# Performance work log

Hardware: AMD Instinct MI355X
Metric: run time of the kernel (lower is better)

The kernel has to match this reference:

```python
import jax, jax.numpy as jnp
import numpy as np

B, N, K = 8, 2048, 32
WIDTH = 20.0      # histogram bin width in degrees
NUM_BINS = 9
EPS = 1e-12       # F.normalize eps


def _knn_idx(pts, k):
    """pts: (B,N,3) -> (B,N,k) indices of k nearest neighbors (incl. self).
    Matches dgcnn.pytorch knn: topk of negative squared distance."""
    d2 = jnp.sum(pts * pts, axis=-1)                       # (B,N)
    neg = 2.0 * jnp.einsum('bnd,bmd->bnm', pts, pts) - d2[:, :, None] - d2[:, None, :]
    _, idx = jax.lax.top_k(neg, k)                         # (B,N,k)
    return idx


def _gather_nn(feat, idx):
    """feat: (B,N,C), idx: (B,N,k) -> (B,N,k,C) per-batch gather."""
    return jax.vmap(lambda f, i: f[i])(feat, idx)


def setup_inputs() -> dict:
    key = jax.random.key(0)
    x = jax.random.normal(key, (B, 3, N), dtype=jnp.float32)
    return {"x": x, "k": K}


def reference(x, k):
    """Faithful JAX port of compute_hog_1x1. x: (B,3,N) -> (B,18,N)."""
    b, _, n = x.shape
    pts = jnp.transpose(x, (0, 2, 1))                      # (B,N,3)
    idx = _knn_idx(pts, k)                                 # (B,N,k)

    x_nn = _gather_nn(pts, idx)                            # (B,N,k,3)
    centered = x_nn - x_nn.mean(axis=2, keepdims=True)

    # Batched SVD; the original detaches (numpy round-trip) -> stop_gradient.
    _, s, vh = jnp.linalg.svd(centered, full_matrices=False)  # s:(B,N,3) vh:(B,N,3,3)
    vh = jax.lax.stop_gradient(vh)
    s = jax.lax.stop_gradient(jnp.sqrt(s))
    gradients = vh[:, :, 0]                                # (B,N,3) principal direction
    magnitudes = s[:, :, 0:1]                              # (B,N,1)

    g_nn = _gather_nn(gradients, idx)                      # (B,N,k,3)
    m_nn = _gather_nn(magnitudes, idx)                     # (B,N,k,1)

    rad2deg = 180.0 / np.pi
    zenith = jnp.arccos(g_nn[..., 2]) * rad2deg            # (B,N,k)
    azimuth = jnp.arctan(g_nn[..., 1] / g_nn[..., 0]) * rad2deg
    # .int() cast in torch truncates toward zero
    ang = jnp.stack([zenith, azimuth], axis=-1).astype(jnp.int32).astype(x.dtype)
    ang = jnp.where(ang < 0, ang + 180.0, ang)             # (B,N,k,2)

    bins = jnp.floor(ang / WIDTH - 0.5) % NUM_BINS         # (B,N,k,2) float
    first_centers = WIDTH * ((bins + 1.0) % NUM_BINS + 0.5)
    first_votes = m_nn * ((first_centers - ang) % 180.0) / WIDTH
    second_centers = WIDTH * (bins + 0.5)
    second_votes = m_nn * ((ang - second_centers) % 180.0) / WIDTH

    bi = bins.astype(jnp.int32)                            # (B,N,k,2)
    oh1 = jax.nn.one_hot(bi, NUM_BINS, dtype=x.dtype)      # (B,N,k,2,9)
    oh2 = jax.nn.one_hot((bi + 1) % NUM_BINS, NUM_BINS, dtype=x.dtype)
    # histogram[:, :, c] += first where bins==c; histogram[:, :, (c+1)%9] += second
    hist = (jnp.einsum('bnkc,bnkcq->bnqc', first_votes, oh1)
            + jnp.einsum('bnkc,bnkcq->bnqc', second_votes, oh2))  # (B,N,9,2)

    # F.normalize(p=2, dim=2)
    norm = jnp.sqrt(jnp.sum(hist * hist, axis=2, keepdims=True))
    hist = hist / jnp.maximum(norm, EPS)

    # torch .view(B, -1, N): flat row-major reinterpret -> (B,18,N)
    return hist.reshape(b, 2 * NUM_BINS, n)
```

## Files before the change

kernel.cpp:

```cpp
#include <hip/hip_runtime.h>
#include <math.h>

#define BB 8
#define NN 2048
#define KK 32

__device__ __forceinline__ float fadd(float a, float b){ return __fadd_rn(a, b); }
__device__ __forceinline__ float fsub(float a, float b){ return __fsub_rn(a, b); }
__device__ __forceinline__ float fmul(float a, float b){ return __fmul_rn(a, b); }
__device__ __forceinline__ float fdiv(float a, float b){ return __fdiv_rn(a, b); }
__device__ __forceinline__ float fsqrtf32(float a){ return __fsqrt_rn(a); }

__device__ float slapy2f(float x, float y) {
    float xa = fabsf(x), ya = fabsf(y);
    float w = fmaxf(xa, ya), z = fminf(xa, ya);
    if (z == 0.0f) return w;
    float q = fdiv(z, w);
    return fmul(w, fsqrtf32(fmaf(q, q, 1.0f)));
}

__device__ void slartgf(float f, float g, float& c, float& s, float& r) {
    if (g == 0.0f) { c = 1.0f; s = 0.0f; r = f; }
    else if (f == 0.0f) { c = 0.0f; s = copysignf(1.0f, g); r = fabsf(g); }
    else {
        float d = fsqrtf32(fmaf(f, f, fmul(g, g)));
        c = fdiv(fabsf(f), d);
        r = copysignf(d, f);
        s = fdiv(g, r);
    }
}

__device__ void slas2f(float f, float g, float h, float& ssmin, float& ssmax) {
    float fa = fabsf(f), ga = fabsf(g), ha = fabsf(h);
    float fhmn = fminf(fa, ha), fhmx = fmaxf(fa, ha);
    if (fhmn == 0.0f) {
        ssmin = 0.0f;
        if (fhmx == 0.0f) ssmax = ga;
        else {
            float mx = fmaxf(fhmx, ga), mn = fminf(fhmx, ga);
            float q = fdiv(mn, mx);
            ssmax = fmul(mx, fsqrtf32(fmaf(q, q, 1.0f)));
        }
    } else {
        if (ga < fhmx) {
            float as = fadd(1.0f, fdiv(fhmn, fhmx));
            float at = fdiv(fsub(fhmx, fhmn), fhmx);
            float q = fdiv(ga, fhmx); float au = fmul(q, q);
            float c = fdiv(2.0f, fadd(fsqrtf32(fmaf(as, as, au)),
                                      fsqrtf32(fmaf(at, at, au))));
            ssmin = fmul(fhmn, c); ssmax = fdiv(fhmx, c);
        } else {
            float au = fdiv(fhmx, ga);
            if (au == 0.0f) { ssmin = fdiv(fmul(fhmn, fhmx), ga); ssmax = ga; }
            else {
                float as = fadd(1.0f, fdiv(fhmn, fhmx));
                float at = fdiv(fsub(fhmx, fhmn), fhmx);
                float t1 = fmul(as, au), t2 = fmul(at, au);
                float c = fdiv(1.0f, fadd(fsqrtf32(fmaf(t1, t1, 1.0f)),
                                          fsqrtf32(fmaf(t2, t2, 1.0f))));
                ssmin = fmul(fmul(fhmn, c), au); ssmin = fadd(ssmin, ssmin);
                ssmax = fdiv(ga, fadd(c, c));
            }
        }
    }
}

__device__ void slasv2f(float f, float g, float h,
                        float& ssmin, float& ssmax,
                        float& snr, float& csr, float& snl, float& csl) {
    const float eps = 5.9604644775390625e-08f;
    float ft = f, fa = fabsf(f), ht = h, ha = fabsf(h);
    int pmax = 1;
    bool swp = (ha > fa);
    if (swp) { pmax = 3; float t = ft; ft = ht; ht = t; t = fa; fa = ha; ha = t; }
    float gt = g, ga = fabsf(gt);
    float clt = 0.f, crt = 0.f, slt = 0.f, srt = 0.f;
    if (ga == 0.0f) {
        ssmin = ha; ssmax = fa; clt = 1.0f; crt = 1.0f; slt = 0.0f; srt = 0.0f;
    } else {
        bool gasmal = true;
        if (ga > fa) {
            pmax = 2;
            if (fdiv(fa, ga) < eps) {
                gasmal = false;
                ssmax = ga;
                ssmin = (ha > 1.0f) ? fdiv(fa, fdiv(ga, ha)) : fmul(fdiv(fa, ga), ha);
                clt = 1.0f; slt = fdiv(ht, gt); srt = 1.0f; crt = fdiv(ft, gt);
            }
        }
        if (gasmal) {
            float dd = fsub(fa, ha);
            float l = (dd == fa) ? 1.0f : fdiv(dd, fa);
            float mm = fdiv(gt, ft);
            float t = fsub(2.0f, l);
            float m2 = fmul(mm, mm);
            float s = fsqrtf32(fmaf(t, t, m2));
            float r = (l == 0.0f) ? fabsf(mm) : fsqrtf32(fmaf(l, l, m2));
            float a = fmul(0.5f, fadd(s, r));
            ssmin = fdiv(ha, a);
            ssmax = fmul(fa, a);
            if (m2 == 0.0f) {
                t = (l == 0.0f) ? fmul(copysignf(2.0f, ft), copysignf(1.0f, gt))
                                : fadd(fdiv(gt, copysignf(dd, ft)), fdiv(mm, t));
            } else {
                t = fmul(fadd(fdiv(mm, fadd(s, t)), fdiv(mm, fadd(r, l))), fadd(1.0f, a));
            }
            float l2 = fsqrtf32(fmaf(t, t, 4.0f));
            crt = fdiv(2.0f, l2); srt = fdiv(t, l2);
            clt = fdiv(fmaf(srt, mm, crt), a);
            slt = fdiv(fmul(fdiv(ht, ft), srt), a);
        }
    }
    if (swp) { csl = srt; snl = crt; csr = slt; snr = clt; }
    else     { csl = clt; snl = slt; csr = crt; snr = srt; }
    float tsign = 0.0f;
    if (pmax == 1) tsign = fmul(fmul(copysignf(1.f, csr), copysignf(1.f, csl)), copysignf(1.f, f));
    if (pmax == 2) tsign = fmul(fmul(copysignf(1.f, snr), copysignf(1.f, csl)), copysignf(1.f, g));
    if (pmax == 3) tsign = fmul(fmul(copysignf(1.f, snr), copysignf(1.f, snl)), copysignf(1.f, h));
    ssmax = copysignf(fabsf(ssmax), tsign);
    ssmin = copysignf(fabsf(ssmin), fmul(tsign, fmul(copysignf(1.f, f), copysignf(1.f, h))));
}

__device__ __forceinline__ void rot_rowsf(float vt[4][4], int lo, int hi, float cc, float ss) {
    #pragma unroll
    for (int c = 1; c <= 3; ++c) {
        float t = vt[hi][c];
        vt[hi][c] = fmaf(cc, t, -fmul(ss, vt[lo][c]));
        vt[lo][c] = fmaf(ss, t, fmul(cc, vt[lo][c]));
    }
}

__device__ void bdsqr3f(float* d, float* e, float vt[4][4]) {
    const float eps  = 5.9604644775390625e-08f;
    const float unfl = 1.1754943508222875e-38f;
    const int n = 3;
    const float tol = fmul(10.0f, eps);
    float thresh;
    {
        float sminoa = fabsf(d[1]);
        if (sminoa != 0.0f) {
            float mu = sminoa;
            for (int i = 2; i <= n; ++i) {
                mu = fmul(fabsf(d[i]), fdiv(mu, fadd(mu, fabsf(e[i - 1]))));
                sminoa = fminf(sminoa, mu);
                if (sminoa == 0.0f) break;
            }
        }
        sminoa = fdiv(sminoa, fsqrtf32(3.0f));
        thresh = fmaxf(fmul(tol, sminoa), fmul(54.0f, unfl));
    }
    int m = n, iter = 0, oldll = -1, oldm = -1, idir = 0;
    float sminl = 0.0f;
    while (m > 1) {
        if (iter > 54) break;
        float smax = fabsf(d[m]);
        int ll = 0; bool split = false;
        for (int lll = 1; lll <= m - 1; ++lll) {
            int l2 = m - lll;
            float abss = fabsf(d[l2]), abse = fabsf(e[l2]);
            if (abse <= thresh) { ll = l2; split = true; break; }
            smax = fmaxf(smax, fmaxf(abss, abse));
        }
        if (split) {
            e[ll] = 0.0f;
            if (ll == m - 1) { m = m - 1; continue; }
            ll = ll + 1;
        } else ll = 1;
        if (ll == m - 1) {
            float sigmn, sigmx, sinr, cosr, sinl, cosl;
            slasv2f(d[m - 1], e[m - 1], d[m], sigmn, sigmx, sinr, cosr, sinl, cosl);
            d[m - 1] = sigmx; e[m - 1] = 0.0f; d[m] = sigmn;
            #pragma unroll
            for (int c = 1; c <= 3; ++c) {
                float t = fmaf(cosr, vt[m - 1][c], fmul(sinr, vt[m][c]));
                vt[m][c] = fmaf(cosr, vt[m][c], -fmul(sinr, vt[m - 1][c]));
                vt[m - 1][c] = t;
            }
            m -= 2; continue;
        }
        if (ll > oldm || m < oldll)
            idir = (fabsf(d[ll]) >= fabsf(d[m])) ? 1 : 2;
        bool deflated = false;
        if (idir == 1) {
            if (fabsf(e[m - 1]) <= fmul(tol, fabsf(d[m]))) { e[m - 1] = 0.0f; continue; }
            float mu = fabsf(d[ll]); sminl = mu;
            for (int lll = ll; lll <= m - 1; ++lll) {
                if (fabsf(e[lll]) <= fmul(tol, mu)) { e[lll] = 0.0f; deflated = true; break; }
                mu = fmul(fabsf(d[lll + 1]), fdiv(mu, fadd(mu, fabsf(e[lll]))));
                sminl = fminf(sminl, mu);
            }
        } else {
            if (fabsf(e[ll]) <= fmul(tol, fabsf(d[ll]))) { e[ll] = 0.0f; continue; }
            float mu = fabsf(d[m]); sminl = mu;
            for (int lll = m - 1; lll >= ll; --lll) {
                if (fabsf(e[lll]) <= fmul(tol, mu)) { e[lll] = 0.0f; deflated = true; break; }
                mu = fmul(fabsf(d[lll]), fdiv(mu, fadd(mu, fabsf(e[lll]))));
                sminl = fminf(sminl, mu);
            }
        }
        if (deflated) continue;
        oldll = ll; oldm = m;
        float shift = 0.0f, rr;
        if (!(fmul(fmul(3.0f, tol), fdiv(sminl, smax)) <= fmaxf(eps, fmul(0.01f, tol)))) {
            float sll;
            if (idir == 1) { sll = fabsf(d[ll]); slas2f(d[m - 1], e[m - 1], d[m], shift, rr); }
            else           { sll = fabsf(d[m]);  slas2f(d[ll], e[ll], d[ll + 1], shift, rr); }
            if (sll > 0.0f) { float q = fdiv(shift, sll); if (fmul(q, q) < eps) shift = 0.0f; }
        }
        iter += m - ll;
        float wc[4], ws[4];
        if (shift == 0.0f) {
            if (idir == 1) {
                float cs = 1.0f, oldcs = 1.0f, sn = 0.0f, oldsn = 0.0f, r2;
                for (int i = ll; i <= m - 1; ++i) {
                    slartgf(fmul(d[i], cs), e[i], cs, sn, r2);
                    if (i > ll) e[i - 1] = fmul(oldsn, r2);
                    slartgf(fmul(oldcs, r2), fmul(d[i + 1], sn), oldcs, oldsn, d[i]);
                    wc[i - ll + 1] = cs; ws[i - ll + 1] = sn;
                }
                float h = fmul(d[m], cs); d[m] = fmul(h, oldcs); e[m - 1] = fmul(h, oldsn);
                if (fabsf(e[m - 1]) <= thresh) e[m - 1] = 0.0f;
                for (int j = 1; j <= m - ll; ++j) rot_rowsf(vt, ll + j - 1, ll + j, wc[j], ws[j]);
            } else {
                float cs = 1.0f, oldcs = 1.0f, sn = 0.0f, oldsn = 0.0f, r2;
                for (int i = m; i >= ll + 1; --i) {
                    slartgf(fmul(d[i], cs), e[i - 1], cs, sn, r2);
                    if (i < m) e[i] = fmul(oldsn, r2);
                    slartgf(fmul(oldcs, r2), fmul(d[i - 1], sn), oldcs, oldsn, d[i]);
                    wc[i - ll] = oldcs; ws[i - ll] = -oldsn;
                }
                float h = fmul(d[ll], cs); d[ll] = fmul(h, oldcs); e[ll] = fmul(h, oldsn);
                if (fabsf(e[ll]) <= thresh) e[ll] = 0.0f;
                for (int j = m - ll; j >= 1; --j) rot_rowsf(vt, ll + j - 1, ll + j, wc[j], ws[j]);
            }
        } else {
            if (idir == 1) {
                float fq = fmul(fsub(fabsf(d[ll]), shift),
                                fadd(copysignf(1.0f, d[ll]), fdiv(shift, d[ll])));
                float g = e[ll], cosr, sinr, cosl, sinl, r2;
                for (int i = ll; i <= m - 1; ++i) {
                    slartgf(fq, g, cosr, sinr, r2);
                    if (i > ll) e[i - 1] = r2;
                    float di = d[i], ei = e[i], dip = d[i + 1];
                    fq         = fmaf(cosr, di, fmul(sinr, ei));
                    float ei_n = fmaf(cosr, ei, -fmul(sinr, di));
                    g = fmul(sinr, dip);
                    float dip_n = fmul(cosr, dip);
                    slartgf(fq, g, cosl, sinl, r2);
                    d[i] = r2;
                    fq       = fmaf(cosl, ei_n, fmul(sinl, dip_n));
                    d[i + 1] = fmaf(cosl, dip_n, -fmul(sinl, ei_n));
                    e[i] = ei_n;
                    if (i < m - 1) { g = fmul(sinl, e[i + 1]); e[i + 1] = fmul(cosl, e[i + 1]); }
                    wc[i - ll + 1] = cosr; ws[i - ll + 1] = sinr;
                }
                e[m - 1] = fq;
                if (fabsf(e[m - 1]) <= thresh) e[m - 1] = 0.0f;
                for (int j = 1; j <= m - ll; ++j) rot_rowsf(vt, ll + j - 1, ll + j, wc[j], ws[j]);
            } else {
                float fq = fmul(fsub(fabsf(d[m]), shift),
                                fadd(copysignf(1.0f, d[m]), fdiv(shift, d[m])));
                float g = e[m - 1], cosr, sinr, cosl, sinl, r2;
                for (int i = m; i >= ll + 1; --i) {
                    slartgf(fq, g, cosr, sinr, r2);
                    if (i < m) e[i] = r2;
                    float di = d[i], em = e[i - 1], dim = d[i - 1];
                    fq         = fmaf(cosr, di, fmul(sinr, em));
                    float em_n = fmaf(cosr, em, -fmul(sinr, di));
                    g = fmul(sinr, dim);
                    float dim_n = fmul(cosr, dim);
                    slartgf(fq, g, cosl, sinl, r2);
                    d[i] = r2;
                    fq       = fmaf(cosl, em_n, fmul(sinl, dim_n));
                    d[i - 1] = fmaf(cosl, dim_n, -fmul(sinl, em_n));
                    e[i - 1] = em_n;
                    if (i > ll + 1) { g = fmul(sinl, e[i - 2]); e[i - 2] = fmul(cosl, e[i - 2]); }
                    wc[i - ll] = cosl; ws[i - ll] = -sinl;
                }
                e[ll] = fq;
                if (fabsf(e[ll]) <= thresh) e[ll] = 0.0f;
                for (int j = m - ll; j >= 1; --j) rot_rowsf(vt, ll + j - 1, ll + j, wc[j], ws[j]);
            }
        }
    }
    for (int i = 1; i <= n; ++i) {
        if (d[i] < 0.0f) {
            d[i] = -d[i];
            for (int c = 1; c <= 3; ++c) vt[i][c] = -vt[i][c];
        }
    }
    for (int i = 1; i <= n - 1; ++i) {
        int isub = 1; float smin2 = d[1];
        for (int j = 2; j <= n + 1 - i; ++j)
            if (d[j] <= smin2) { isub = j; smin2 = d[j]; }
        int tgt = n + 1 - i;
        if (isub != tgt) {
            d[isub] = d[tgt]; d[tgt] = smin2;
            for (int c = 1; c <= 3; ++c) { float t = vt[isub][c]; vt[isub][c] = vt[tgt][c]; vt[tgt][c] = t; }
        }
    }
}

__global__ void d2_kernel(const float* __restrict__ x, float* __restrict__ d2) {
    int t = blockIdx.x * blockDim.x + threadIdx.x;
    if (t >= BB * NN) return;
    int b = t / NN, n = t % NN;
    const float* xb = x + b * 3 * NN;
    float xv = xb[n], yv = xb[NN + n], zv = xb[2 * NN + n];
    d2[t] = fadd(fadd(fmul(xv, xv), fmul(yv, yv)), fmul(zv, zv));
}

__device__ __forceinline__ unsigned int f32_sortable(float f) {
    unsigned int b = __float_as_uint(f);
    return b ^ ((unsigned int)((int)b >> 31) | 0x80000000u);
}
__device__ __forceinline__ float sortable_f32(unsigned int s) {
    unsigned int b = s ^ (~(unsigned int)((int)s >> 31) | 0x80000000u);
    return __uint_as_float(b);
}

template <int CTRL, int RM>
__device__ __forceinline__ unsigned long long dpp_umax64(unsigned long long k) {
    int nhi = __builtin_amdgcn_update_dpp(0, (int)(unsigned int)(k >> 32), CTRL, RM, 0xF, false);
    int nlo = __builtin_amdgcn_update_dpp(0, (int)(unsigned int)k,         CTRL, RM, 0xF, false);
    unsigned long long nk = ((unsigned long long)(unsigned int)nhi << 32) | (unsigned int)nlo;
    return nk > k ? nk : k;
}

__device__ __forceinline__ unsigned long long pop_best(unsigned int (&vals)[32], int lane) {
    unsigned int m = vals[0];
    #pragma unroll
    for (int s = 1; s < 32; ++s) m = (vals[s] > m) ? vals[s] : m;
    int bs = 0;
    #pragma unroll
    for (int s = 31; s >= 0; --s) if (vals[s] == m) bs = s;
    #pragma unroll
    for (int s = 0; s < 32; ++s) vals[s] = (s == bs) ? 0u : vals[s];
    int j = bs * 64 + lane;
    return ((unsigned long long)m << 32) | (unsigned int)(2047 - j);
}

__global__ void __launch_bounds__(256) knn_kernel(const float* __restrict__ x,
                                                  const float* __restrict__ d2,
                                                  int* __restrict__ idx) {
    int lane = threadIdx.x & 63;
    int wid  = threadIdx.x >> 6;
    int row  = blockIdx.x * 4 + wid;
    int b = row / NN, i = row % NN;
    const float* xb  = x  + b * 3 * NN;
    const float* d2b = d2 + b * NN;

    float xi = xb[i], yi = xb[NN + i], zi = xb[2 * NN + i];
    float d2i = d2b[i];

    unsigned int vals[32];
    #pragma unroll
    for (int s = 0; s < 32; ++s) {
        int j = s * 64 + lane;
        float dot = fmul(xi, xb[j]);
        dot = fmaf(yi, xb[NN + j], dot);
        dot = fmaf(zi, xb[2 * NN + j], dot);
        float v = fsub(fsub(fmul(2.0f, dot), d2i), d2b[j]);
        vals[s] = f32_sortable(v);
    }

    unsigned long long l0 = pop_best(vals, lane);
    unsigned long long l1 = pop_best(vals, lane);
    unsigned long long l2 = pop_best(vals, lane);
    unsigned long long l3 = pop_best(vals, lane);

    int* idxrow = idx + row * KK;
    unsigned int c1v = 0, c2v = 0, c3v = 0, c31v = 0, c32v = 0;
    int c1i = 0, c2i = 0, c3i = 0, c31i = 0, c32i = 0;

    #pragma unroll 1
    for (int t = 0; t < KK + 1; ++t) {
        if (__any(l0 == 0ull)) {
            bool need = (l0 == 0ull);
            unsigned int m = vals[0];
            #pragma unroll
            for (int s = 1; s < 32; ++s) m = (vals[s] > m) ? vals[s] : m;
            int bs = 0;
            #pragma unroll
            for (int s = 31; s >= 0; --s) if (vals[s] == m) bs = s;
            #pragma unroll
            for (int s = 0; s < 32; ++s)
                vals[s] = (need && s == bs) ? 0u : vals[s];
            unsigned long long ent = ((unsigned long long)m << 32)
                                   | (unsigned int)(2047 - (bs * 64 + lane));
            l0 = need ? ent : l0;
        }

        unsigned long long k = l0;
        k = dpp_umax64<0x111, 0xF>(k);
        k = dpp_umax64<0x112, 0xF>(k);
        k = dpp_umax64<0x114, 0xF>(k);
        k = dpp_umax64<0x118, 0xF>(k);
        k = dpp_umax64<0x142, 0xA>(k);
        k = dpp_umax64<0x143, 0xC>(k);

        unsigned int wbest = (unsigned int)__builtin_amdgcn_readlane((int)(k >> 32), 63);
        unsigned int wlow  = (unsigned int)__builtin_amdgcn_readlane((int)(k & 0xFFFFFFFFull), 63);
        int wj = 2047 - (int)(wlow & 0x7FFu);

        bool amw = ((unsigned int)l0 == wlow);
        l0 = amw ? l1 : l0;
        l1 = amw ? l2 : l1;
        l2 = amw ? l3 : l2;
        l3 = amw ? 0ull : l3;

        if (t == 1)           { c1v = wbest;  c1i = wj; }
        else if (t == 2)      { c2v = wbest;  c2i = wj; }
        else if (t == 3)      { c3v = wbest;  c3i = wj; }
        else if (t == KK - 1) { c31v = wbest; c31i = wj; }
        else if (t == KK)     { c32v = wbest; c32i = wj; }
        else if (lane == 0)   idxrow[t] = wj;
    }

    if (lane == 0) {
        const float TIE = 4e-7f;
        float r1  = sortable_f32(c1v),  r2  = sortable_f32(c2v), r3 = sortable_f32(c3v);
        float r31 = sortable_f32(c31v), r32 = sortable_f32(c32v);
        if (fabsf(r1 - r2) < TIE) { int ti = c1i; c1i = c2i; c2i = ti; float tv = r1; r1 = r2; r2 = tv; }
        if (fabsf(r2 - r3) < TIE) { int ti = c2i; c2i = c3i; c3i = ti; float tv = r2; r2 = r3; r3 = tv; }
        idxrow[1] = c1i; idxrow[2] = c2i; idxrow[3] = c3i;
        idxrow[KK - 1] = (fabsf(r31 - r32) < TIE) ? c32i : c31i;
    }
}

__global__ void eig_kernel(const float* __restrict__ x, const int* __restrict__ idx,
                           float* __restrict__ grad, float* __restrict__ mag) {
    int t = blockIdx.x * blockDim.x + threadIdx.x;
    if (t >= BB * NN) return;
    int b = t / NN;
    const float* xb = x + b * 3 * NN;
    const int* id = idx + t * KK;

    float A[KK][3];
    float s0 = 0.f, s1 = 0.f, s2 = 0.f;
    #pragma unroll
    for (int j = 0; j < KK; ++j) {
        int n = id[j];
        s0 = fadd(s0, xb[n]); s1 = fadd(s1, xb[NN + n]); s2 = fadd(s2, xb[2 * NN + n]);
    }
    float m0 = fdiv(s0, 32.f), m1 = fdiv(s1, 32.f), m2 = fdiv(s2, 32.f);
    #pragma unroll
    for (int j = 0; j < KK; ++j) {
        int n = id[j];
        A[j][0] = fsub(xb[n], m0);
        A[j][1] = fsub(xb[NN + n], m1);
        A[j][2] = fsub(xb[2 * NN + n], m2);
    }

    #pragma unroll
    for (int i = 0; i < 3; ++i) {
        float alpha = A[i][i];
        double nacc = 0.0;
        #pragma unroll
        for (int r = i + 1; r < KK; ++r) nacc += (double)A[r][i] * (double)A[r][i];
        float xnorm = (float)sqrt(nacc);
        if (xnorm != 0.0f) {
            float beta = -copysignf(slapy2f(alpha, xnorm), alpha);
            float tau  = fdiv(fsub(beta, alpha), beta);
            float scal = fdiv(1.0f, fsub(alpha, beta));
            #pragma unroll
            for (int r = i + 1; r < KK; ++r) A[r][i] = fmul(A[r][i], scal);
            A[i][i] = beta;
            #pragma unroll
            for (int j = i + 1; j < 3; ++j) {
                float acc = 0.0f;
                #pragma unroll
                for (int r = i + 1; r < KK; ++r) acc = fmaf(A[r][i], A[r][j], acc);
                float w = fadd(acc, A[i][j]);
                A[i][j] = fmaf(-tau, w, A[i][j]);
                float temp = fmul(-tau, w);
                #pragma unroll
                for (int r = i + 1; r < KK; ++r) A[r][j] = fmaf(A[r][i], temp, A[r][j]);
            }
        }
    }
    float B11 = A[0][0], B12 = A[0][1], B13 = A[0][2];
    float B22 = A[1][1], B23 = A[1][2], B33 = A[2][2];

    float d[4], e[3];
    float taup = 0.0f, v2p = 0.0f;
    d[1] = B11;
    float B32 = 0.0f;
    if (B13 != 0.0f) {
        float xn = fsqrtf32(fmul(B13, B13));
        float beta = -copysignf(slapy2f(B12, xn), B12);
        taup = fdiv(fsub(beta, B12), beta);
        float scal = fdiv(1.0f, fsub(B12, beta));
        v2p = fmul(B13, scal);
        e[1] = beta;
        float w2 = fadd(fmul(B23, v2p), B22);
        float w3 = fmul(B33, v2p);
        B22 = fmaf(-taup, w2, B22);
        B32 = fmul(-taup, w3);
        float tmp = fmul(-taup, v2p);
        B23 = fmaf(w2, tmp, B23);
        B33 = fmaf(w3, tmp, B33);
    } else e[1] = B12;
    if (B32 != 0.0f) {
        float xn = fsqrtf32(fmul(B32, B32));
        float beta = -copysignf(slapy2f(B22, xn), B22);
        float tauq = fdiv(fsub(beta, B22), beta);
        float scal = fdiv(1.0f, fsub(B22, beta));
        float v2 = fmul(B32, scal);
        d[2] = beta;
        float w = fadd(fmul(v2, B33), B23);
        B23 = fmaf(-tauq, w, B23);
        float tmp = fmul(-tauq, w);
        B33 = fmaf(v2, tmp, B33);
    } else d[2] = B22;
    e[2] = B23;
    d[3] = B33;

    float vt[4][4];
    for (int r = 1; r <= 3; ++r)
        for (int c = 1; c <= 3; ++c) vt[r][c] = (r == c) ? 1.0f : 0.0f;
    bdsqr3f(d, e, vt);

    if (taup != 0.0f) {
        float tmp = fmul(-taup, v2p);
        for (int r = 1; r <= 3; ++r) {
            float w = fadd(fmul(vt[r][3], v2p), vt[r][2]);
            vt[r][2] = fmaf(-taup, w, vt[r][2]);
            vt[r][3] = fmaf(w, tmp, vt[r][3]);
        }
    }

    int im = 1;
    if (d[2] > d[im]) im = 2;
    if (d[3] > d[im]) im = 3;
    grad[t * 3 + 0] = vt[im][1];
    grad[t * 3 + 1] = vt[im][2];
    grad[t * 3 + 2] = vt[im][3];
    mag[t] = fsqrtf32(d[im]);
}

__global__ void vote_kernel(const float* __restrict__ grad, const float* __restrict__ mag,
                            float4* __restrict__ votes, int* __restrict__ binsq) {
    int t = blockIdx.x * blockDim.x + threadIdx.x;
    if (t >= BB * NN) return;
    const float r2d = (float)(180.0 / M_PI);

    float gx = grad[t * 3 + 0];
    float gy = grad[t * 3 + 1];
    float gz = grad[t * 3 + 2];
    float m  = mag[t];

    float zen = (float)acos((double)gz);
    float zd  = fmul(zen, r2d);
    float q0  = fdiv(gy, gx);
    float azr = (float)atan((double)q0);
    float ad  = fmul(azr, r2d);

    float a0 = (zd != zd) ? -2147483648.0f : (float)(int)zd;
    float a1 = (ad != ad) ? -2147483648.0f : (float)(int)ad;

    float v1s[2], v2s[2]; int bis[2];
    #pragma unroll
    for (int c = 0; c < 2; ++c) {
        float a = (c == 0) ? a0 : a1;
        if (a < 0.0f) a = fadd(a, 180.0f);
        float tq = fdiv(a, 20.0f);
        float t2 = fsub(tq, 0.5f);
        float fb = floorf(t2);
        float bin = fmodf(fb, 9.0f); if (bin != 0.0f && bin < 0.0f) bin = fadd(bin, 9.0f);
        float b1 = fadd(bin, 1.0f);
        float b1m = fmodf(b1, 9.0f);
        float fc = fmul(20.0f, fadd(b1m, 0.5f));
        float df = fsub(fc, a);
        float rm = fmodf(df, 180.0f); if (rm != 0.0f && rm < 0.0f) rm = fadd(rm, 180.0f);
        v1s[c] = fdiv(fmul(m, rm), 20.0f);
        float sc = fmul(20.0f, fadd(bin, 0.5f));
        float ds = fsub(a, sc);
        float rm2 = fmodf(ds, 180.0f); if (rm2 != 0.0f && rm2 < 0.0f) rm2 = fadd(rm2, 180.0f);
        v2s[c] = fdiv(fmul(m, rm2), 20.0f);
        bis[c] = (int)bin;
    }
    votes[t] = make_float4(v1s[0], v2s[0], v1s[1], v2s[1]);
    binsq[t] = bis[0] | (bis[1] << 8);
}

__global__ void hist_kernel(const int* __restrict__ idx, const float4* __restrict__ votes,
                            const int* __restrict__ binsq, float* __restrict__ out) {
    int t = blockIdx.x * blockDim.x + threadIdx.x;
    if (t >= BB * NN) return;
    int b = t / NN, n = t % NN;
    const int* id = idx + t * KK;

    float h1[9][2], h2[9][2];
    #pragma unroll
    for (int q = 0; q < 9; ++q) { h1[q][0] = h1[q][1] = 0.f; h2[q][0] = h2[q][1] = 0.f; }

    for (int j = 0; j < KK; ++j) {
        int jj = b * NN + id[j];
        float4 v = votes[jj];
        int bp = binsq[jj];
        int bi0 = bp & 0xFF, bi1 = bp >> 8;
        int b20 = bi0 + 1; if (b20 >= 9) b20 -= 9;
        h1[bi0][0] = fadd(h1[bi0][0], v.x);
        h2[b20][0] = fadd(h2[b20][0], v.y);
        int b21 = bi1 + 1; if (b21 >= 9) b21 -= 9;
        h1[bi1][1] = fadd(h1[bi1][1], v.z);
        h2[b21][1] = fadd(h2[b21][1], v.w);
    }

    float* o = out + b * (18 * NN) + n * 18;
    #pragma unroll
    for (int c = 0; c < 2; ++c) {
        float hist[9];
        #pragma unroll
        for (int q = 0; q < 9; ++q) hist[q] = fadd(h1[q][c], h2[q][c]);
        float acc = 0.0f;
        #pragma unroll
        for (int q = 0; q < 9; ++q) acc = fadd(acc, fmul(hist[q], hist[q]));
        float nr = fsqrtf32(acc);
        float den = fmaxf(nr, 1e-12f);
        #pragma unroll
        for (int q = 0; q < 9; ++q) o[q * 2 + c] = fdiv(hist[q], den);
    }
}

extern "C" void kernel_launch(void* const* d_in, const int* in_sizes, int n_in,
                              void* d_out, int out_size, void* d_ws, size_t ws_size,
                              hipStream_t stream) {
    const float* x = (const float*)d_in[0];
    float* out = (float*)d_out;

    char* ws = (char*)d_ws;
    size_t off = 0;
    int* idx = (int*)(ws + off);        off += (size_t)BB * NN * KK * sizeof(int);
    float* d2 = (float*)(ws + off);     off += (size_t)BB * NN * sizeof(float);
    float* grad = (float*)(ws + off);   off += (size_t)BB * NN * 3 * sizeof(float);
    float* mag = (float*)(ws + off);    off += (size_t)BB * NN * sizeof(float);
    float4* votes = (float4*)(ws + off); off += (size_t)BB * NN * sizeof(float4);
    int* binsq = (int*)(ws + off);

    d2_kernel  <<<(BB * NN + 63) / 64, 64, 0, stream>>>(x, d2);
    knn_kernel <<<BB * NN / 4, 256, 0, stream>>>(x, d2, idx);
    eig_kernel <<<(BB * NN + 63) / 64, 64, 0, stream>>>(x, idx, grad, mag);
    vote_kernel<<<(BB * NN + 63) / 64, 64, 0, stream>>>(grad, mag, votes, binsq);
    hist_kernel<<<(BB * NN + 63) / 64, 64, 0, stream>>>(idx, votes, binsq, out);
}
```

Measured before the change: 189.3 us.

## Keep SVD state in registers, fuse vote into eig kernel, predicate histogram updates

Replaces the dynamically indexed d/e/vt arrays in the 3x3 bidiagonal SVD with named scalars and select-based accessors, so they can stay in registers instead of spilling to scratch memory. Merges the vote kernel into the eig kernel, which removes one launch and the grad/mag round trip through global memory. The histogram kernel now updates bins through unrolled predicated selects rather than dynamic indexing, which keeps the histogram arrays in registers at the cost of more ALU work per neighbor.

```diff
diff --git a/kernel.cpp b/kernel.cpp
--- a/kernel.cpp
+++ b/kernel.cpp
@@ -121,80 +121,117 @@
     ssmin = copysignf(fabsf(ssmin), fmul(tsign, fmul(copysignf(1.f, f), copysignf(1.f, h))));
 }
 
-__device__ __forceinline__ void rot_rowsf(float vt[4][4], int lo, int hi, float cc, float ss) {
-    #pragma unroll
-    for (int c = 1; c <= 3; ++c) {
-        float t = vt[hi][c];
-        vt[hi][c] = fmaf(cc, t, -fmul(ss, vt[lo][c]));
-        vt[lo][c] = fmaf(ss, t, fmul(cc, vt[lo][c]));
-    }
-}
-
-__device__ void bdsqr3f(float* d, float* e, float vt[4][4]) {
+struct VT3 {
+    float a11, a12, a13, a21, a22, a23, a31, a32, a33;
+    template<int C> __device__ __forceinline__ float get(int r) const {
+        if (C == 1) return r == 1 ? a11 : (r == 2 ? a21 : a31);
+        if (C == 2) return r == 1 ? a12 : (r == 2 ? a22 : a32);
+        return r == 1 ? a13 : (r == 2 ? a23 : a33);
+    }
+    template<int C> __device__ __forceinline__ void set(int r, float x) {
+        if (C == 1)      { if (r == 1) a11 = x; else if (r == 2) a21 = x; else a31 = x; }
+        else if (C == 2) { if (r == 1) a12 = x; else if (r == 2) a22 = x; else a32 = x; }
+        else             { if (r == 1) a13 = x; else if (r == 2) a23 = x; else a33 = x; }
+    }
+};
+
+template<int C>
+__device__ __forceinline__ void rot_col(VT3& vt, int lo, int hi, float cc, float ss) {
+    float t   = vt.get<C>(hi);
+    float vlo = vt.get<C>(lo);
+    vt.set<C>(hi, fmaf(cc, t, -fmul(ss, vlo)));
+    vt.set<C>(lo, fmaf(ss, t, fmul(cc, vlo)));
+}
+__device__ __forceinline__ void rot_rowsf(VT3& vt, int lo, int hi, float cc, float ss) {
+    rot_col<1>(vt, lo, hi, cc, ss);
+    rot_col<2>(vt, lo, hi, cc, ss);
+    rot_col<3>(vt, lo, hi, cc, ss);
+}
+
+template<int C>
+__device__ __forceinline__ void rot_sv(VT3& vt, int m, float cosr, float sinr) {
+    float vm1 = vt.get<C>(m - 1), vm = vt.get<C>(m);
+    float t = fmaf(cosr, vm1, fmul(sinr, vm));
+    vt.set<C>(m, fmaf(cosr, vm, -fmul(sinr, vm1)));
+    vt.set<C>(m - 1, t);
+}
+
+template<int C>
+__device__ __forceinline__ void swap_rows_col(VT3& vt, int r1, int r2) {
+    float t = vt.get<C>(r1);
+    vt.set<C>(r1, vt.get<C>(r2));
+    vt.set<C>(r2, t);
+}
+
+__device__ void bdsqr3f(float& d1, float& d2, float& d3,
+                        float& e1, float& e2, VT3& vt) {
     const float eps  = 5.9604644775390625e-08f;
     const float unfl = 1.1754943508222875e-38f;
-    const int n = 3;
     const float tol = fmul(10.0f, eps);
+
+    auto dget = [&](int i) -> float { return i == 1 ? d1 : (i == 2 ? d2 : d3); };
+    auto dset = [&](int i, float x) { if (i == 1) d1 = x; else if (i == 2) d2 = x; else d3 = x; };
+    auto eget = [&](int i) -> float { return i == 1 ? e1 : e2; };
+    auto eset = [&](int i, float x) { if (i == 1) e1 = x; else e2 = x; };
+
     float thresh;
     {
-        float sminoa = fabsf(d[1]);
+        float sminoa = fabsf(d1);
         if (sminoa != 0.0f) {
             float mu = sminoa;
-            for (int i = 2; i <= n; ++i) {
-                mu = fmul(fabsf(d[i]), fdiv(mu, fadd(mu, fabsf(e[i - 1]))));
+            mu = fmul(fabsf(d2), fdiv(mu, fadd(mu, fabsf(e1))));
+            sminoa = fminf(sminoa, mu);
+            if (sminoa != 0.0f) {
+                mu = fmul(fabsf(d3), fdiv(mu, fadd(mu, fabsf(e2))));
                 sminoa = fminf(sminoa, mu);
-                if (sminoa == 0.0f) break;
             }
         }
         sminoa = fdiv(sminoa, fsqrtf32(3.0f));
         thresh = fmaxf(fmul(tol, sminoa), fmul(54.0f, unfl));
     }
-    int m = n, iter = 0, oldll = -1, oldm = -1, idir = 0;
+    int m = 3, iter = 0, oldll = -1, oldm = -1, idir = 0;
     float sminl = 0.0f;
     while (m > 1) {
         if (iter > 54) break;
-        float smax = fabsf(d[m]);
+        float smax = fabsf(dget(m));
         int ll = 0; bool split = false;
         for (int lll = 1; lll <= m - 1; ++lll) {
             int l2 = m - lll;
-            float abss = fabsf(d[l2]), abse = fabsf(e[l2]);
+            float abss = fabsf(dget(l2)), abse = fabsf(eget(l2));
             if (abse <= thresh) { ll = l2; split = true; break; }
             smax = fmaxf(smax, fmaxf(abss, abse));
         }
         if (split) {
-            e[ll] = 0.0f;
+            eset(ll, 0.0f);
             if (ll == m - 1) { m = m - 1; continue; }
             ll = ll + 1;
         } else ll = 1;
         if (ll == m - 1) {
             float sigmn, sigmx, sinr, cosr, sinl, cosl;
-            slasv2f(d[m - 1], e[m - 1], d[m], sigmn, sigmx, sinr, cosr, sinl, cosl);
-            d[m - 1] = sigmx; e[m - 1] = 0.0f; d[m] = sigmn;
-            #pragma unroll
-            for (int c = 1; c <= 3; ++c) {
-                float t = fmaf(cosr, vt[m - 1][c], fmul(sinr, vt[m][c]));
-                vt[m][c] = fmaf(cosr, vt[m][c], -fmul(sinr, vt[m - 1][c]));
-                vt[m - 1][c] = t;
-            }
+            slasv2f(dget(m - 1), eget(m - 1), dget(m), sigmn, sigmx, sinr, cosr, sinl, cosl);
+            dset(m - 1, sigmx); eset(m - 1, 0.0f); dset(m, sigmn);
+            rot_sv<1>(vt, m, cosr, sinr);
+            rot_sv<2>(vt, m, cosr, sinr);
+            rot_sv<3>(vt, m, cosr, sinr);
             m -= 2; continue;
         }
         if (ll > oldm || m < oldll)
-            idir = (fabsf(d[ll]) >= fabsf(d[m])) ? 1 : 2;
+            idir = (fabsf(dget(ll)) >= fabsf(dget(m))) ? 1 : 2;
         bool deflated = false;
         if (idir == 1) {
-            if (fabsf(e[m - 1]) <= fmul(tol, fabsf(d[m]))) { e[m - 1] = 0.0f; continue; }
-            float mu = fabsf(d[ll]); sminl = mu;
+            if (fabsf(eget(m - 1)) <= fmul(tol, fabsf(dget(m)))) { eset(m - 1, 0.0f); continue; }
+            float mu = fabsf(dget(ll)); sminl = mu;
             for (int lll = ll; lll <= m - 1; ++lll) {
-                if (fabsf(e[lll]) <= fmul(tol, mu)) { e[lll] = 0.0f; deflated = true; break; }
-                mu = fmul(fabsf(d[lll + 1]), fdiv(mu, fadd(mu, fabsf(e[lll]))));
+                if (fabsf(eget(lll)) <= fmul(tol, mu)) { eset(lll, 0.0f); deflated = true; break; }
+                mu = fmul(fabsf(dget(lll + 1)), fdiv(mu, fadd(mu, fabsf(eget(lll)))));
                 sminl = fminf(sminl, mu);
             }
         } else {
-            if (fabsf(e[ll]) <= fmul(tol, fabsf(d[ll]))) { e[ll] = 0.0f; continue; }
-            float mu = fabsf(d[m]); sminl = mu;
+            if (fabsf(eget(ll)) <= fmul(tol, fabsf(dget(ll)))) { eset(ll, 0.0f); continue; }
+            float mu = fabsf(dget(m)); sminl = mu;
             for (int lll = m - 1; lll >= ll; --lll) {
-                if (fabsf(e[lll]) <= fmul(tol, mu)) { e[lll] = 0.0f; deflated = true; break; }
-                mu = fmul(fabsf(d[lll]), fdiv(mu, fadd(mu, fabsf(e[lll]))));
+                if (fabsf(eget(lll)) <= fmul(tol, mu)) { eset(lll, 0.0f); deflated = true; break; }
+                mu = fmul(fabsf(dget(lll)), fdiv(mu, fadd(mu, fabsf(eget(lll)))));
                 sminl = fminf(sminl, mu);
             }
         }
@@ -203,100 +240,107 @@
         float shift = 0.0f, rr;
         if (!(fmul(fmul(3.0f, tol), fdiv(sminl, smax)) <= fmaxf(eps, fmul(0.01f, tol)))) {
             float sll;
-            if (idir == 1) { sll = fabsf(d[ll]); slas2f(d[m - 1], e[m - 1], d[m], shift, rr); }
-            else           { sll = fabsf(d[m]);  slas2f(d[ll], e[ll], d[ll + 1], shift, rr); }
+            if (idir == 1) { sll = fabsf(dget(ll)); slas2f(dget(m - 1), eget(m - 1), dget(m), shift, rr); }
+            else           { sll = fabsf(dget(m));  slas2f(dget(ll), eget(ll), dget(ll + 1), shift, rr); }
             if (sll > 0.0f) { float q = fdiv(shift, sll); if (fmul(q, q) < eps) shift = 0.0f; }
         }
         iter += m - ll;
-        float wc[4], ws[4];
+        float wc1 = 0.f, wc2 = 0.f, ws1 = 0.f, ws2 = 0.f;
+        auto wcset = [&](int j, float x) { if (j == 1) wc1 = x; else wc2 = x; };
+        auto wsset = [&](int j, float x) { if (j == 1) ws1 = x; else ws2 = x; };
+        auto wcget = [&](int j) -> float { return j == 1 ? wc1 : wc2; };
+        auto wsget = [&](int j) -> float { return j == 1 ? ws1 : ws2; };
         if (shift == 0.0f) {
             if (idir == 1) {
                 float cs = 1.0f, oldcs = 1.0f, sn = 0.0f, oldsn = 0.0f, r2;
                 for (int i = ll; i <= m - 1; ++i) {
-                    slartgf(fmul(d[i], cs), e[i], cs, sn, r2);
-                    if (i > ll) e[i - 1] = fmul(oldsn, r2);
-                    slartgf(fmul(oldcs, r2), fmul(d[i + 1], sn), oldcs, oldsn, d[i]);
-                    wc[i - ll + 1] = cs; ws[i - ll + 1] = sn;
+                    slartgf(fmul(dget(i), cs), eget(i), cs, sn, r2);
+                    if (i > ll) eset(i - 1, fmul(oldsn, r2));
+                    float td;
+                    slartgf(fmul(oldcs, r2), fmul(dget(i + 1), sn), oldcs, oldsn, td);
+                    dset(i, td);
+                    wcset(i - ll + 1, cs); wsset(i - ll + 1, sn);
                 }
-                float h = fmul(d[m], cs); d[m] = fmul(h, oldcs); e[m - 1] = fmul(h, oldsn);
-                if (fabsf(e[m - 1]) <= thresh) e[m - 1] = 0.0f;
-                for (int j = 1; j <= m - ll; ++j) rot_rowsf(vt, ll + j - 1, ll + j, wc[j], ws[j]);
+                float h = fmul(dget(m), cs); dset(m, fmul(h, oldcs)); eset(m - 1, fmul(h, oldsn));
+                if (fabsf(eget(m - 1)) <= thresh) eset(m - 1, 0.0f);
+                for (int j = 1; j <= m - ll; ++j) rot_rowsf(vt, ll + j - 1, ll + j, wcget(j), wsget(j));
             } else {
                 float cs = 1.0f, oldcs = 1.0f, sn = 0.0f, oldsn = 0.0f, r2;
                 for (int i = m; i >= ll + 1; --i) {
-                    slartgf(fmul(d[i], cs), e[i - 1], cs, sn, r2);
-                    if (i < m) e[i] = fmul(oldsn, r2);
-                    slartgf(fmul(oldcs, r2), fmul(d[i - 1], sn), oldcs, oldsn, d[i]);
-                    wc[i - ll] = oldcs; ws[i - ll] = -oldsn;
+                    slartgf(fmul(dget(i), cs), eget(i - 1), cs, sn, r2);
+                    if (i < m) eset(i, fmul(oldsn, r2));
+                    float td;
+                    slartgf(fmul(oldcs, r2), fmul(dget(i - 1), sn), oldcs, oldsn, td);
+                    dset(i, td);
+                    wcset(i - ll, oldcs); wsset(i - ll, -oldsn);
                 }
-                float h = fmul(d[ll], cs); d[ll] = fmul(h, oldcs); e[ll] = fmul(h, oldsn);
-                if (fabsf(e[ll]) <= thresh) e[ll] = 0.0f;
-                for (int j = m - ll; j >= 1; --j) rot_rowsf(vt, ll + j - 1, ll + j, wc[j], ws[j]);
+                float h = fmul(dget(ll), cs); dset(ll, fmul(h, oldcs)); eset(ll, fmul(h, oldsn));
+                if (fabsf(eget(ll)) <= thresh) eset(ll, 0.0f);
+                for (int j = m - ll; j >= 1; --j) rot_rowsf(vt, ll + j - 1, ll + j, wcget(j), wsget(j));
             }
         } else {
             if (idir == 1) {
-                float fq = fmul(fsub(fabsf(d[ll]), shift),
-                                fadd(copysignf(1.0f, d[ll]), fdiv(shift, d[ll])));
-                float g = e[ll], cosr, sinr, cosl, sinl, r2;
+                float fq = fmul(fsub(fabsf(dget(ll)), shift),
+                                fadd(copysignf(1.0f, dget(ll)), fdiv(shift, dget(ll))));
+                float g = eget(ll), cosr, sinr, cosl, sinl, r2;
                 for (int i = ll; i <= m - 1; ++i) {
                     slartgf(fq, g, cosr, sinr, r2);
-                    if (i > ll) e[i - 1] = r2;
-                    float di = d[i], ei = e[i], dip = d[i + 1];
+                    if (i > ll) eset(i - 1, r2);
+                    float di = dget(i), ei = eget(i), dip = dget(i + 1);
                     fq         = fmaf(cosr, di, fmul(sinr, ei));
                     float ei_n = fmaf(cosr, ei, -fmul(sinr, di));
                     g = fmul(sinr, dip);
                     float dip_n = fmul(cosr, dip);
                     slartgf(fq, g, cosl, sinl, r2);
-                    d[i] = r2;
-                    fq       = fmaf(cosl, ei_n, fmul(sinl, dip_n));
-                    d[i + 1] = fmaf(cosl, dip_n, -fmul(sinl, ei_n));
-                    e[i] = ei_n;
-                    if (i < m - 1) { g = fmul(sinl, e[i + 1]); e[i + 1] = fmul(cosl, e[i + 1]); }
-                    wc[i - ll + 1] = cosr; ws[i - ll + 1] = sinr;
+                    dset(i, r2);
+                    fq = fmaf(cosl, ei_n, fmul(sinl, dip_n));
+                    dset(i + 1, fmaf(cosl, dip_n, -fmul(sinl, ei_n)));
+                    eset(i, ei_n);
+                    if (i < m - 1) { float eo = eget(i + 1); g = fmul(sinl, eo); eset(i + 1, fmul(cosl, eo)); }
+                    wcset(i - ll + 1, cosr); wsset(i - ll + 1, sinr);
                 }
-                e[m - 1] = fq;
-                if (fabsf(e[m - 1]) <= thresh) e[m - 1] = 0.0f;
-                for (int j = 1; j <= m - ll; ++j) rot_rowsf(vt, ll + j - 1, ll + j, wc[j], ws[j]);
+                eset(m - 1, fq);
+                if (fabsf(eget(m - 1)) <= thresh) eset(m - 1, 0.0f);
+                for (int j = 1; j <= m - ll; ++j) rot_rowsf(vt, ll + j - 1, ll + j, wcget(j), wsget(j));
             } else {
-                float fq = fmul(fsub(fabsf(d[m]), shift),
-                                fadd(copysignf(1.0f, d[m]), fdiv(shift, d[m])));
-                float g = e[m - 1], cosr, sinr, cosl, sinl, r2;
+                float fq = fmul(fsub(fabsf(dget(m)), shift),
+                                fadd(copysignf(1.0f, dget(m)), fdiv(shift, dget(m))));
+                float g = eget(m - 1), cosr, sinr, cosl, sinl, r2;
                 for (int i = m; i >= ll + 1; --i) {
                     slartgf(fq, g, cosr, sinr, r2);
-                    if (i < m) e[i] = r2;
-                    float di = d[i], em = e[i - 1], dim = d[i - 1];
+                    if (i < m) eset(i, r2);
+                    float di = dget(i), em = eget(i - 1), dim = dget(i - 1);
                     fq         = fmaf(cosr, di, fmul(sinr, em));
                     float em_n = fmaf(cosr, em, -fmul(sinr, di));
                     g = fmul(sinr, dim);
                     float dim_n = fmul(cosr, dim);
                     slartgf(fq, g, cosl, sinl, r2);
-                    d[i] = r2;
-                    fq       = fmaf(cosl, em_n, fmul(sinl, dim_n));
-                    d[i - 1] = fmaf(cosl, dim_n, -fmul(sinl, em_n));
-                    e[i - 1] = em_n;
-                    if (i > ll + 1) { g = fmul(sinl, e[i - 2]); e[i - 2] = fmul(cosl, e[i - 2]); }
-                    wc[i - ll] = cosl; ws[i - ll] = -sinl;
+                    dset(i, r2);
+                    fq = fmaf(cosl, em_n, fmul(sinl, dim_n));
+                    dset(i - 1, fmaf(cosl, dim_n, -fmul(sinl, em_n)));
+                    eset(i - 1, em_n);
+                    if (i > ll + 1) { float eo = eget(i - 2); g = fmul(sinl, eo); eset(i - 2, fmul(cosl, eo)); }
+                    wcset(i - ll, cosl); wsset(i - ll, -sinl);
                 }
-                e[ll] = fq;
-                if (fabsf(e[ll]) <= thresh) e[ll] = 0.0f;
-                for (int j = m - ll; j >= 1; --j) rot_rowsf(vt, ll + j - 1, ll + j, wc[j], ws[j]);
-            }
-        }
-    }
-    for (int i = 1; i <= n; ++i) {
-        if (d[i] < 0.0f) {
-            d[i] = -d[i];
-            for (int c = 1; c <= 3; ++c) vt[i][c] = -vt[i][c];
-        }
-    }
-    for (int i = 1; i <= n - 1; ++i) {
-        int isub = 1; float smin2 = d[1];
-        for (int j = 2; j <= n + 1 - i; ++j)
-            if (d[j] <= smin2) { isub = j; smin2 = d[j]; }
-        int tgt = n + 1 - i;
+                eset(ll, fq);
+                if (fabsf(eget(ll)) <= thresh) eset(ll, 0.0f);
+                for (int j = m - ll; j >= 1; --j) rot_rowsf(vt, ll + j - 1, ll + j, wcget(j), wsget(j));
+            }
+        }
+    }
+    if (d1 < 0.0f) { d1 = -d1; vt.a11 = -vt.a11; vt.a12 = -vt.a12; vt.a13 = -vt.a13; }
+    if (d2 < 0.0f) { d2 = -d2; vt.a21 = -vt.a21; vt.a22 = -vt.a22; vt.a23 = -vt.a23; }
+    if (d3 < 0.0f) { d3 = -d3; vt.a31 = -vt.a31; vt.a32 = -vt.a32; vt.a33 = -vt.a33; }
+    for (int i = 1; i <= 2; ++i) {
+        int isub = 1; float smin2 = d1;
+        for (int j = 2; j <= 4 - i; ++j)
+            if (dget(j) <= smin2) { isub = j; smin2 = dget(j); }
+        int tgt = 4 - i;
         if (isub != tgt) {
-            d[isub] = d[tgt]; d[tgt] = smin2;
-            for (int c = 1; c <= 3; ++c) { float t = vt[isub][c]; vt[isub][c] = vt[tgt][c]; vt[tgt][c] = t; }
+            dset(isub, dget(tgt)); dset(tgt, smin2);
+            swap_rows_col<1>(vt, isub, tgt);
+            swap_rows_col<2>(vt, isub, tgt);
+            swap_rows_col<3>(vt, isub, tgt);
         }
     }
 }
@@ -429,7 +473,7 @@
 }
 
 __global__ void eig_kernel(const float* __restrict__ x, const int* __restrict__ idx,
-                           float* __restrict__ grad, float* __restrict__ mag) {
+                           float4* __restrict__ votes, int* __restrict__ binsq) {
     int t = blockIdx.x * blockDim.x + threadIdx.x;
     if (t >= BB * NN) return;
     int b = t / NN;
@@ -482,9 +526,9 @@
     float B11 = A[0][0], B12 = A[0][1], B13 = A[0][2];
     float B22 = A[1][1], B23 = A[1][2], B33 = A[2][2];
 
-    float d[4], e[3];
+    float d1v, d2v, d3v, e1v, e2v;
     float taup = 0.0f, v2p = 0.0f;
-    d[1] = B11;
+    d1v = B11;
     float B32 = 0.0f;
     if (B13 != 0.0f) {
         float xn = fsqrtf32(fmul(B13, B13));
@@ -492,7 +536,7 @@
         taup = fdiv(fsub(beta, B12), beta);
         float scal = fdiv(1.0f, fsub(B12, beta));
         v2p = fmul(B13, scal);
-        e[1] = beta;
+        e1v = beta;
         float w2 = fadd(fmul(B23, v2p), B22);
         float w3 = fmul(B33, v2p);
         B22 = fmaf(-taup, w2, B22);
@@ -500,56 +544,51 @@
         float tmp = fmul(-taup, v2p);
         B23 = fmaf(w2, tmp, B23);
         B33 = fmaf(w3, tmp, B33);
-    } else e[1] = B12;
+    } else e1v = B12;
     if (B32 != 0.0f) {
         float xn = fsqrtf32(fmul(B32, B32));
         float beta = -copysignf(slapy2f(B22, xn), B22);
         float tauq = fdiv(fsub(beta, B22), beta);
         float scal = fdiv(1.0f, fsub(B22, beta));
         float v2 = fmul(B32, scal);
-        d[2] = beta;
+        d2v = beta;
         float w = fadd(fmul(v2, B33), B23);
         B23 = fmaf(-tauq, w, B23);
         float tmp = fmul(-tauq, w);
         B33 = fmaf(v2, tmp, B33);
-    } else d[2] = B22;
-    e[2] = B23;
-    d[3] = B33;
-
-    float vt[4][4];
-    for (int r = 1; r <= 3; ++r)
-        for (int c = 1; c <= 3; ++c) vt[r][c] = (r == c) ? 1.0f : 0.0f;
-    bdsqr3f(d, e, vt);
+    } else d2v = B22;
+    e2v = B23;
+    d3v = B33;
+
+    VT3 vt;
+    vt.a11 = 1.0f; vt.a12 = 0.0f; vt.a13 = 0.0f;
+    vt.a21 = 0.0f; vt.a22 = 1.0f; vt.a23 = 0.0f;
+    vt.a31 = 0.0f; vt.a32 = 0.0f; vt.a33 = 1.0f;
+    bdsqr3f(d1v, d2v, d3v, e1v, e2v, vt);
 
     if (taup != 0.0f) {
         float tmp = fmul(-taup, v2p);
-        for (int r = 1; r <= 3; ++r) {
-            float w = fadd(fmul(vt[r][3], v2p), vt[r][2]);
-            vt[r][2] = fmaf(-taup, w, vt[r][2]);
-            vt[r][3] = fmaf(w, tmp, vt[r][3]);
-        }
+        { float w = fadd(fmul(vt.a13, v2p), vt.a12);
+          vt.a12 = fmaf(-taup, w, vt.a12);
+          vt.a13 = fmaf(w, tmp, vt.a13); }
+        { float w = fadd(fmul(vt.a23, v2p), vt.a22);
+          vt.a22 = fmaf(-taup, w, vt.a22);
+          vt.a23 = fmaf(w, tmp, vt.a23); }
+        { float w = fadd(fmul(vt.a33, v2p), vt.a32);
+          vt.a32 = fmaf(-taup, w, vt.a32);
+          vt.a33 = fmaf(w, tmp, vt.a33); }
     }
 
     int im = 1;
-    if (d[2] > d[im]) im = 2;
-    if (d[3] > d[im]) im = 3;
-    grad[t * 3 + 0] = vt[im][1];
-    grad[t * 3 + 1] = vt[im][2];
-    grad[t * 3 + 2] = vt[im][3];
-    mag[t] = fsqrtf32(d[im]);
-}
-
-__global__ void vote_kernel(const float* __restrict__ grad, const float* __restrict__ mag,
-                            float4* __restrict__ votes, int* __restrict__ binsq) {
-    int t = blockIdx.x * blockDim.x + threadIdx.x;
-    if (t >= BB * NN) return;
+    if (d2v > d1v) im = 2;
+    float dcur = (im == 2) ? d2v : d1v;
+    if (d3v > dcur) im = 3;
+    float gx = vt.get<1>(im);
+    float gy = vt.get<2>(im);
+    float gz = vt.get<3>(im);
+    float m  = fsqrtf32((im == 1) ? d1v : ((im == 2) ? d2v : d3v));
+
     const float r2d = (float)(180.0 / M_PI);
-
-    float gx = grad[t * 3 + 0];
-    float gy = grad[t * 3 + 1];
-    float gz = grad[t * 3 + 2];
-    float m  = mag[t];
-
     float zen = (float)acos((double)gz);
     float zd  = fmul(zen, r2d);
     float q0  = fdiv(gy, gx);
@@ -601,11 +640,14 @@
         int bp = binsq[jj];
         int bi0 = bp & 0xFF, bi1 = bp >> 8;
         int b20 = bi0 + 1; if (b20 >= 9) b20 -= 9;
-        h1[bi0][0] = fadd(h1[bi0][0], v.x);
-        h2[b20][0] = fadd(h2[b20][0], v.y);
         int b21 = bi1 + 1; if (b21 >= 9) b21 -= 9;
-        h1[bi1][1] = fadd(h1[bi1][1], v.z);
-        h2[b21][1] = fadd(h2[b21][1], v.w);
+        #pragma unroll
+        for (int q = 0; q < 9; ++q) {
+            h1[q][0] = (bi0 == q) ? fadd(h1[q][0], v.x) : h1[q][0];
+            h2[q][0] = (b20 == q) ? fadd(h2[q][0], v.y) : h2[q][0];
+            h1[q][1] = (bi1 == q) ? fadd(h1[q][1], v.z) : h1[q][1];
+            h2[q][1] = (b21 == q) ? fadd(h2[q][1], v.w) : h2[q][1];
+        }
     }
 
     float* o = out + b * (18 * NN) + n * 18;
@@ -632,16 +674,13 @@
 
     char* ws = (char*)d_ws;
     size_t off = 0;
-    int* idx = (int*)(ws + off);        off += (size_t)BB * NN * KK * sizeof(int);
-    float* d2 = (float*)(ws + off);     off += (size_t)BB * NN * sizeof(float);
-    float* grad = (float*)(ws + off);   off += (size_t)BB * NN * 3 * sizeof(float);
-    float* mag = (float*)(ws + off);    off += (size_t)BB * NN * sizeof(float);
+    int* idx = (int*)(ws + off);         off += (size_t)BB * NN * KK * sizeof(int);
+    float* d2 = (float*)(ws + off);      off += (size_t)BB * NN * sizeof(float);
     float4* votes = (float4*)(ws + off); off += (size_t)BB * NN * sizeof(float4);
     int* binsq = (int*)(ws + off);
 
     d2_kernel  <<<(BB * NN + 63) / 64, 64, 0, stream>>>(x, d2);
     knn_kernel <<<BB * NN / 4, 256, 0, stream>>>(x, d2, idx);
-    eig_kernel <<<(BB * NN + 63) / 64, 64, 0, stream>>>(x, idx, grad, mag);
-    vote_kernel<<<(BB * NN + 63) / 64, 64, 0, stream>>>(grad, mag, votes, binsq);
+    eig_kernel <<<(BB * NN + 63) / 64, 64, 0, stream>>>(x, idx, votes, binsq);
     hist_kernel<<<(BB * NN + 63) / 64, 64, 0, stream>>>(idx, votes, binsq, out);
 }
```

Result: faster. 185.6 us (-2.0%).
